# Performance work log

Measured on AMD Instinct MI355X. Metric: run time of the kernel, lower is better.

The kernel has to match this reference:

```python
import jax, jax.numpy as jnp
from jax import lax
import numpy as np

B, T, D_IN = 4, 1024, 8
D_MODEL, N_LAYERS, HORIZON, D_OUT = 512, 2, 24, 8
D_STATE, D_CONV, EXPAND = 64, 4, 2
D_INNER = EXPAND * D_MODEL
DT_RANK = -(-D_MODEL // 16)  # ceil(d_model/16) = 32
LN_EPS = 1e-5


def setup_inputs() -> dict:
    key = jax.random.key(0)
    ks = iter(jax.random.split(key, 24))
    rn = lambda shape, s: jax.random.normal(next(ks), shape, jnp.float32) * s
    A_log = jnp.tile(jnp.log(jnp.arange(1, D_STATE + 1, dtype=jnp.float32)), (N_LAYERS, D_INNER, 1))
    return {
        "x": rn((B, T, D_IN), 1.0),
        "W_in": rn((D_IN, D_MODEL), 0.3), "b_in": jnp.zeros((D_MODEL,), jnp.float32),
        "W_xz": rn((N_LAYERS, D_MODEL, 2 * D_INNER), 0.04),
        "conv_w": rn((N_LAYERS, D_INNER, D_CONV), 0.3), "conv_b": jnp.zeros((N_LAYERS, D_INNER), jnp.float32),
        "W_xproj": rn((N_LAYERS, D_INNER, DT_RANK + 2 * D_STATE), 0.03),
        "W_dt": rn((N_LAYERS, DT_RANK, D_INNER), 0.1), "b_dt": rn((N_LAYERS, D_INNER), 0.1) - 4.0,
        "A_log": A_log, "D_skip": jnp.ones((N_LAYERS, D_INNER), jnp.float32),
        "W_out": rn((N_LAYERS, D_INNER, D_MODEL), 0.03),
        "ln_g": jnp.ones((D_MODEL,), jnp.float32), "ln_b": jnp.zeros((D_MODEL,), jnp.float32),
        "W_h1": rn((D_MODEL, D_MODEL), 0.04), "b_h1": jnp.zeros((D_MODEL,), jnp.float32),
        "W_h2": rn((D_MODEL, HORIZON * D_OUT), 0.04), "b_h2": jnp.zeros((HORIZON * D_OUT,), jnp.float32),
    }


def mamba_block(h, Wxz, cw, cb, Wxp, Wdt, bdt, Alog, Dsk, Wout):
    # h: [B,T,d_model] -> [B,T,d_model]  (mamba-ssm Mamba block, no residual)
    xz = h @ Wxz                                   # [B,T,2*d_inner]
    xb, z = jnp.split(xz, 2, axis=-1)
    # depthwise causal conv over time
    xc = jnp.transpose(xb, (0, 2, 1))              # [B,d_inner,T]
    xc = lax.conv_general_dilated(xc, cw[:, None, :], (1,), [(D_CONV - 1, 0)],
                                  feature_group_count=D_INNER)
    xc = jax.nn.silu(xc + cb[None, :, None])
    xc = jnp.transpose(xc, (0, 2, 1))              # [B,T,d_inner]
    # input-dependent dt, B, C
    xdb = xc @ Wxp                                 # [B,T,dt_rank+2*d_state]
    dt_r = xdb[..., :DT_RANK]
    Bc = xdb[..., DT_RANK:DT_RANK + D_STATE]
    Cc = xdb[..., DT_RANK + D_STATE:]
    dt = jax.nn.softplus(dt_r @ Wdt + bdt)         # [B,T,d_inner]
    A = -jnp.exp(Alog)                             # [d_inner,d_state]

    def step(hst, ins):
        dt_t, B_t, C_t, x_t = ins                  # [B,d_inner],[B,N],[B,N],[B,d_inner]
        dA = jnp.exp(dt_t[..., None] * A)          # [B,d_inner,N]
        hst = dA * hst + dt_t[..., None] * B_t[:, None, :] * x_t[..., None]
        y = jnp.einsum('bdn,bn->bd', hst, C_t)
        return hst, y

    h0 = jnp.zeros((h.shape[0], D_INNER, D_STATE), h.dtype)
    xs = (jnp.transpose(dt, (1, 0, 2)), jnp.transpose(Bc, (1, 0, 2)),
          jnp.transpose(Cc, (1, 0, 2)), jnp.transpose(xc, (1, 0, 2)))
    _, ys = lax.scan(step, h0, xs)                 # ys: [T,B,d_inner]
    y = jnp.transpose(ys, (1, 0, 2)) + Dsk * xc
    y = y * jax.nn.silu(z)
    return y @ Wout


def reference(x, W_in, b_in, W_xz, conv_w, conv_b, W_xproj, W_dt, b_dt, A_log, D_skip,
              W_out, ln_g, ln_b, W_h1, b_h1, W_h2, b_h2):
    h = x @ W_in + b_in                            # [B,T,d_model]
    for i in range(N_LAYERS):
        h = mamba_block(h, W_xz[i], conv_w[i], conv_b[i], W_xproj[i], W_dt[i],
                        b_dt[i], A_log[i], D_skip[i], W_out[i])
    mu = jnp.mean(h, axis=-1, keepdims=True)
    var = jnp.mean(jnp.square(h - mu), axis=-1, keepdims=True)
    h = (h - mu) * lax.rsqrt(var + LN_EPS) * ln_g + ln_b
    last = h[:, -1, :]                             # [B,d_model]
    hid = jax.nn.gelu(last @ W_h1 + b_h1, approximate=False)
    yhat = hid @ W_h2 + b_h2                       # [B,horizon*d_out]
    return yhat.reshape(x.shape[0], HORIZON, D_OUT)
```

## Files before the change

kernel.cpp:

```cpp
#include <hip/hip_runtime.h>
#include <hip/hip_bf16.h>

static constexpr int kB      = 4;
static constexpr int kT      = 1024;
static constexpr int kDIN    = 8;
static constexpr int kDMODEL = 512;
static constexpr int kNLAYER = 2;
static constexpr int kHOR    = 24;
static constexpr int kDOUT   = 8;
static constexpr int kDSTATE = 64;
static constexpr int kDINNER = 1024;
static constexpr int kDTRANK = 32;
static constexpr int kXPROJ  = 160;
static constexpr int kXPAD   = 256;
static constexpr int kBT     = kB * kT;

typedef __bf16 bf16x8 __attribute__((ext_vector_type(8)));
typedef float  f32x4  __attribute__((ext_vector_type(4)));

__device__ __forceinline__ float silu_f(float x)     { return x / (1.f + __expf(-x)); }
__device__ __forceinline__ float softplus_f(float x) { return (x > 20.f) ? x : log1pf(__expf(x)); }
__device__ __forceinline__ float gelu_f(float x)     { return 0.5f * x * (1.f + erff(x * 0.70710678118654752f)); }

__device__ __forceinline__ void gld_lds16(const void* g, void* l) {
    __builtin_amdgcn_global_load_lds(
        (const __attribute__((address_space(1))) unsigned int*)g,
        (__attribute__((address_space(3))) unsigned int*)l, 16, 0, 0);
}

__device__ __forceinline__ float readlane_f(float v, int l) {
    return __int_as_float(__builtin_amdgcn_readlane(__float_as_int(v), l));
}
template<int CTRL>
__device__ __forceinline__ float dpp_mov(float v) {
    return __int_as_float(__builtin_amdgcn_update_dpp(
        0, __float_as_int(v), CTRL, 0xf, 0xf, false));
}

__global__ __launch_bounds__(256) void wtrans_kernel(
    const float* __restrict__ in, int K, int N, int in_lstride,
    __hip_bfloat16* __restrict__ out, int Kpad, int out_lstride)
{
    __shared__ float tile[32][33];
    const int tid = threadIdx.x;
    const int n0 = blockIdx.x * 32;
    const int k0 = blockIdx.y * 32;
    const float* inl = in + (size_t)blockIdx.z * in_lstride;
    __hip_bfloat16* outl = out + (size_t)blockIdx.z * out_lstride;

#pragma unroll
    for (int p = 0; p < 4; ++p) {
        int idx = p * 256 + tid;
        int ki = idx >> 5, ni = idx & 31;
        float v = 0.f;
        if (k0 + ki < K && n0 + ni < N) v = inl[(size_t)(k0 + ki) * N + n0 + ni];
        tile[ki][ni] = v;
    }
    __syncthreads();
#pragma unroll
    for (int p = 0; p < 4; ++p) {
        int idx = p * 256 + tid;
        int ni = idx >> 5, ki = idx & 31;
        outl[(size_t)(n0 + ni) * Kpad + k0 + ki] = __float2bfloat16(tile[ki][ni]);
    }
}

template<int MODE>
__global__ __launch_bounds__(256) void mfma_gemm_bt(
    const __hip_bfloat16* __restrict__ A, int lda,
    const __hip_bfloat16* __restrict__ BT, int ldb,
    const float* __restrict__ bias,
    float* __restrict__ C, int ldc,
    void* __restrict__ C2,
    int K)
{
    __shared__ __align__(16) __hip_bfloat16 sA[128][64];
    __shared__ __align__(16) __hip_bfloat16 sB[128][64];

    const int tid  = threadIdx.x;
    const int lane = tid & 63;
    const int w    = tid >> 6;
    const int wm   = w >> 1, wn = w & 1;
    const int m0   = blockIdx.y * 128;
    const int n0   = blockIdx.x * 128;

    f32x4 acc[4][4] = {};

    const int lrow = lane & 15;
    const int lk   = (lane >> 4) << 3;

    const int grow = tid >> 3;
    const int gcol = (tid & 7) * 8;
    char* ldsA = (char*)&sA[0][0] + w * 1024;
    char* ldsB = (char*)&sB[0][0] + w * 1024;

    for (int k0 = 0; k0 < K; k0 += 64) {
        __syncthreads();
#pragma unroll
        for (int p = 0; p < 4; ++p) {
            gld_lds16(A  + (size_t)(m0 + grow + p * 32) * lda + k0 + gcol, ldsA + p * 4096);
            gld_lds16(BT + (size_t)(n0 + grow + p * 32) * ldb + k0 + gcol, ldsB + p * 4096);
        }
        __syncthreads();
#pragma unroll
        for (int ks = 0; ks < 2; ++ks) {
            bf16x8 af[4], bfr[4];
#pragma unroll
            for (int i = 0; i < 4; ++i) {
                af[i]  = *reinterpret_cast<const bf16x8*>(&sA[wm * 64 + i * 16 + lrow][ks * 32 + lk]);
                bfr[i] = *reinterpret_cast<const bf16x8*>(&sB[wn * 64 + i * 16 + lrow][ks * 32 + lk]);
            }
#pragma unroll
            for (int i = 0; i < 4; ++i)
#pragma unroll
                for (int j = 0; j < 4; ++j)
                    acc[i][j] = __builtin_amdgcn_mfma_f32_16x16x32_bf16(af[i], bfr[j], acc[i][j], 0, 0, 0);
        }
    }

    const int crow = (lane >> 4) * 4;
    const int ccol = lane & 15;
#pragma unroll
    for (int i = 0; i < 4; ++i) {
#pragma unroll
        for (int j = 0; j < 4; ++j) {
#pragma unroll
            for (int r = 0; r < 4; ++r) {
                int row = m0 + wm * 64 + i * 16 + crow + r;
                int col = n0 + wn * 64 + j * 16 + ccol;
                float v = acc[i][j][r];
                if (MODE == 1) {
                    C[(size_t)row * ldc + col] = v;
                    ((__hip_bfloat16*)C2)[(size_t)row * ldc + col] = __float2bfloat16(v);
                } else if (MODE == 2) {
                    C[(size_t)row * ldc + col] = softplus_f(v + bias[col]);
                } else {
                    if (col < kDINNER)
                        ((__hip_bfloat16*)C)[(size_t)row * ldc + col] = __float2bfloat16(v);
                    else
                        ((__hip_bfloat16*)C2)[(size_t)row * ldc + (col - kDINNER)] =
                            __float2bfloat16(silu_f(v));
                }
            }
        }
    }
}

__global__ __launch_bounds__(256) void in_proj_kernel(
    const float* __restrict__ x, const float* __restrict__ W,
    const float* __restrict__ b,
    float* __restrict__ h, __hip_bfloat16* __restrict__ hb)
{
    int idx = blockIdx.x * 256 + threadIdx.x;
    int m = idx >> 9, n = idx & 511;
    float acc = b[n];
    const float* xr = x + m * kDIN;
#pragma unroll
    for (int k = 0; k < kDIN; ++k)
        acc = fmaf(xr[k], W[k * kDMODEL + n], acc);
    h[idx]  = acc;
    hb[idx] = __float2bfloat16(acc);
}

__global__ __launch_bounds__(256) void conv_silu_kernel(
    const __hip_bfloat16* __restrict__ xb,
    const float* __restrict__ cw, const float* __restrict__ cb,
    __hip_bfloat16* __restrict__ xc)
{
    int idx = blockIdx.x * 256 + threadIdx.x;
    int d   = idx & (kDINNER - 1);
    int bt  = idx >> 10;
    int t   = bt & (kT - 1);

    float4 wv = *reinterpret_cast<const float4*>(cw + d * 4);
    float acc = cb[d];
    const __hip_bfloat16* base = xb + (size_t)bt * kDINNER + d;
    if (t >= 3) {
        acc = fmaf(__bfloat162float(base[-3 * kDINNER]), wv.x, acc);
        acc = fmaf(__bfloat162float(base[-2 * kDINNER]), wv.y, acc);
        acc = fmaf(__bfloat162float(base[-1 * kDINNER]), wv.z, acc);
        acc = fmaf(__bfloat162float(base[0]),            wv.w, acc);
    } else {
        if (t >= 2) acc = fmaf(__bfloat162float(base[-2 * kDINNER]), wv.y, acc);
        if (t >= 1) acc = fmaf(__bfloat162float(base[-1 * kDINNER]), wv.z, acc);
        acc = fmaf(__bfloat162float(base[0]), wv.w, acc);
    }
    xc[idx] = __float2bfloat16(silu_f(acc));
}

__global__ __launch_bounds__(256, 4) void scan_kernel(
    const float* __restrict__ dt,
    const float* __restrict__ xdb,
    const __hip_bfloat16* __restrict__ xc,
    const __hip_bfloat16* __restrict__ zs,
    const float* __restrict__ Alog,
    const float* __restrict__ Dsk,
    __hip_bfloat16* __restrict__ yg)
{
    __shared__ __align__(16) float sBC[2][32][128];
    __shared__ float sY[2][32][4];

    const int tid  = threadIdx.x;
    const int lane = tid & 63;
    const int w    = tid >> 6;
    const int bb = blockIdx.x;
    const int b  = (bb & 7) >> 1;
    const int d0 = ((bb >> 3) + (bb & 1) * 128) * 4;
    const int d  = d0 + w;

    const float a2  = -__expf(Alog[d * kDSTATE + lane]) * 1.44269504f;
    const float dsk = Dsk[d];
    const size_t rowbase = (size_t)b * kT;
    float s = 0.f;

    auto stage = [&](int c, int buf) {
        const float* src = xdb + (rowbase + c * 32 + w * 8 + (lane >> 5)) * kXPAD
                               + kDTRANK + (lane & 31) * 4;
#pragma unroll
        for (int p = 0; p < 4; ++p)
            gld_lds16(src + p * 2 * kXPAD, &sBC[buf][w * 8 + p * 2][0]);
    };
    auto loadpair = [&](int pr, float& odt, float& oxc, float& odtx) {
        size_t row = rowbase + pr * 64 + lane;
        odt  = dt[row * kDINNER + d];
        oxc  = __bfloat162float(xc[row * kDINNER + d]);
        odtx = odt * oxc;
    };

    float vdt, vxc, vdtx;
    stage(0, 0);
    loadpair(0, vdt, vxc, vdtx);
    __syncthreads();

    for (int pr = 0; pr < kT / 64; ++pr) {
#pragma unroll
        for (int half = 0; half < 2; ++half) {
            const int c   = pr * 2 + half;
            const int buf = half;
            if (c + 1 < kT / 32) stage(c + 1, buf ^ 1);
            float ndt, nxc, ndtx;
            const bool ld = (half == 1) && (pr + 1 < kT / 64);
            if (ld) loadpair(pr + 1, ndt, nxc, ndtx);

            float yv[32];
#pragma unroll
            for (int i = 0; i < 32; ++i) {
                float Bv   = sBC[buf][i][lane];
                float Cv   = sBC[buf][i][64 + lane];
                float sdt  = readlane_f(vdt,  half * 32 + i);
                float sdtx = readlane_f(vdtx, half * 32 + i);
                float dA   = exp2f(sdt * a2);
                s = fmaf(dA, s, sdtx * Bv);
                yv[i] = s * Cv;
            }

#pragma unroll
            for (int m = 0; m < 16; ++m) {
                float av = yv[2 * m], bv = yv[2 * m + 1];
                float cv = (lane & 1) ? bv : av;
                float dv = (lane & 1) ? av : bv;
                yv[m] = cv + dpp_mov<0xB1>(dv);
            }
#pragma unroll
            for (int m = 0; m < 8; ++m) {
                float av = yv[2 * m], bv = yv[2 * m + 1];
                float cv = (lane & 2) ? bv : av;
                float dv = (lane & 2) ? av : bv;
                yv[m] = cv + dpp_mov<0x4E>(dv);
            }
#pragma unroll
            for (int j = 2; j < 5; ++j) {
                const int S = 1 << j;
#pragma unroll
                for (int m = 0; m < (32 >> (j + 1)); ++m) {
                    float av = yv[2 * m], bv = yv[2 * m + 1];
                    float cv = (lane & S) ? bv : av;
                    float dv = (lane & S) ? av : bv;
                    yv[m] = cv + __shfl_xor(dv, S, 64);
                }
            }
            float y = yv[0];
            y += __shfl_xor(y, 32, 64);

            if ((lane & 32) == half * 32)
                sY[buf][lane & 31][w] = fmaf(dsk, vxc, y);
            __syncthreads();

            if (tid < 128) {
                int r = tid >> 2, j2 = tid & 3;
                size_t g = (rowbase + c * 32 + r) * kDINNER + d0 + j2;
                yg[g] = __float2bfloat16(sY[buf][r][j2] * __bfloat162float(zs[g]));
            }
            if (ld) { vdt = ndt; vxc = nxc; vdtx = ndtx; }
        }
    }
}

template<int N, int KK, int ACT>
__global__ __launch_bounds__(256) void head_gemm(
    const float* __restrict__ A,
    const float* __restrict__ B,
    const float* __restrict__ bias,
    float* __restrict__ C)
{
    const int n = blockIdx.x * 64 + (threadIdx.x & 63);
    const int b = threadIdx.x >> 6;
    const float* a  = A + b * KK;
    const float* bp = B + n;
    float acc = 0.f;
#pragma unroll 16
    for (int k = 0; k < KK; ++k)
        acc = fmaf(a[k], bp[(size_t)k * N], acc);
    float v = acc + bias[n];
    if (ACT == 3) v = gelu_f(v);
    C[(size_t)b * N + n] = v;
}

__global__ __launch_bounds__(256) void ln_last_kernel(
    const float* __restrict__ h,
    const float* __restrict__ g, const float* __restrict__ be,
    float* __restrict__ out)
{
    __shared__ float sbuf[8];
    int b = blockIdx.x, tid = threadIdx.x;
    const float* row = h + (size_t)(b * kT + (kT - 1)) * kDMODEL;

    float v0 = row[tid], v1 = row[tid + 256];
    float s = v0 + v1;
    float q = v0 * v0 + v1 * v1;
#pragma unroll
    for (int m = 32; m >= 1; m >>= 1) {
        s += __shfl_xor(s, m, 64);
        q += __shfl_xor(q, m, 64);
    }
    int wid = tid >> 6;
    if ((tid & 63) == 0) { sbuf[wid] = s; sbuf[4 + wid] = q; }
    __syncthreads();
    if (tid == 0) {
        float S = 0.f, Q = 0.f;
        for (int i = 0; i < 4; ++i) { S += sbuf[i]; Q += sbuf[4 + i]; }
        sbuf[0] = S; sbuf[4] = Q;
    }
    __syncthreads();
    float mean = sbuf[0] * (1.f / kDMODEL);
    float var  = sbuf[4] * (1.f / kDMODEL) - mean * mean;
    float inv  = rsqrtf(var + 1e-5f);
    out[b * kDMODEL + tid]       = (v0 - mean) * inv * g[tid]       + be[tid];
    out[b * kDMODEL + tid + 256] = (v1 - mean) * inv * g[tid + 256] + be[tid + 256];
}

extern "C" void kernel_launch(void* const* d_in, const int* in_sizes, int n_in,
                              void* d_out, int out_size, void* d_ws, size_t ws_size,
                              hipStream_t stream)
{
    const float* x      = (const float*)d_in[0];
    const float* W_in   = (const float*)d_in[1];
    const float* b_in   = (const float*)d_in[2];
    const float* W_xz   = (const float*)d_in[3];
    const float* conv_w = (const float*)d_in[4];
    const float* conv_b = (const float*)d_in[5];
    const float* W_xp   = (const float*)d_in[6];
    const float* W_dt   = (const float*)d_in[7];
    const float* b_dt   = (const float*)d_in[8];
    const float* A_log  = (const float*)d_in[9];
    const float* D_skip = (const float*)d_in[10];
    const float* W_out  = (const float*)d_in[11];
    const float* ln_g   = (const float*)d_in[12];
    const float* ln_b   = (const float*)d_in[13];
    const float* W_h1   = (const float*)d_in[14];
    const float* b_h1   = (const float*)d_in[15];
    const float* W_h2   = (const float*)d_in[16];
    const float* b_h2   = (const float*)d_in[17];
    float* out = (float*)d_out;

    char* p = (char*)d_ws;
    auto alloc = [&](size_t bytes) { char* q = p; p += (bytes + 255) & ~(size_t)255; return q; };
    float*          h       = (float*)         alloc((size_t)kBT * kDMODEL * 4);
    __hip_bfloat16* h_bf    = (__hip_bfloat16*)alloc((size_t)kBT * kDMODEL * 2);
    __hip_bfloat16* xb_bf   = (__hip_bfloat16*)alloc((size_t)kBT * kDINNER * 2);
    __hip_bfloat16* z_bf    = (__hip_bfloat16*)alloc((size_t)kBT * kDINNER * 2);
    __hip_bfloat16* xc_bf   = (__hip_bfloat16*)alloc((size_t)kBT * kDINNER * 2);
    float*          xdb     = (float*)         alloc((size_t)kBT * kXPAD * 4);
    __hip_bfloat16* xdb_bf  = (__hip_bfloat16*)alloc((size_t)kBT * kXPAD * 2);
    float*          dtb     = (float*)         alloc((size_t)kBT * kDINNER * 4);
    __hip_bfloat16* ys_bf   = (__hip_bfloat16*)alloc((size_t)kBT * kDINNER * 2);
    __hip_bfloat16* wxz_bt  = (__hip_bfloat16*)alloc((size_t)2 * 2048 * 512 * 2);
    __hip_bfloat16* wxp_bt  = (__hip_bfloat16*)alloc((size_t)2 * 256 * 1024 * 2);
    __hip_bfloat16* wdt_bt  = (__hip_bfloat16*)alloc((size_t)2 * 1024 * 64 * 2);
    __hip_bfloat16* wout_bt = (__hip_bfloat16*)alloc((size_t)2 * 512 * 1024 * 2);
    float*          lnb     = (float*)         alloc(kB * kDMODEL * 4);
    float*          hid     = (float*)         alloc(kB * kDMODEL * 4);

    wtrans_kernel<<<dim3(64, 16, 2), 256, 0, stream>>>(W_xz, 512,  2048, 512 * 2048, wxz_bt,  512,  2048 * 512);
    wtrans_kernel<<<dim3(8,  32, 2), 256, 0, stream>>>(W_xp, 1024, 160,  1024 * 160, wxp_bt,  1024, 256 * 1024);
    wtrans_kernel<<<dim3(32, 2,  2), 256, 0, stream>>>(W_dt, 32,   1024, 32 * 1024,  wdt_bt,  64,   1024 * 64);
    wtrans_kernel<<<dim3(16, 32, 2), 256, 0, stream>>>(W_out, 1024, 512, 1024 * 512, wout_bt, 1024, 512 * 1024);

    in_proj_kernel<<<(kBT * kDMODEL) / 256, 256, 0, stream>>>(x, W_in, b_in, h, h_bf);

    for (int l = 0; l < kNLAYER; ++l) {
        const float* cw_l  = conv_w + (size_t)l * kDINNER * 4;
        const float* cb_l  = conv_b + (size_t)l * kDINNER;
        const float* bdt_l = b_dt   + (size_t)l * kDINNER;
        const float* Al_l  = A_log  + (size_t)l * kDINNER * kDSTATE;
        const float* Dsk_l = D_skip + (size_t)l * kDINNER;
        const __hip_bfloat16* wxz_l  = wxz_bt  + (size_t)l * 2048 * 512;
        const __hip_bfloat16* wxp_l  = wxp_bt  + (size_t)l * 256 * 1024;
        const __hip_bfloat16* wdt_l  = wdt_bt  + (size_t)l * 1024 * 64;
        const __hip_bfloat16* wout_l = wout_bt + (size_t)l * 512 * 1024;

        mfma_gemm_bt<4><<<dim3(16, 32), 256, 0, stream>>>(
            h_bf, kDMODEL, wxz_l, 512, nullptr, (float*)xb_bf, kDINNER, z_bf, kDMODEL);
        conv_silu_kernel<<<(kBT * kDINNER) / 256, 256, 0, stream>>>(xb_bf, cw_l, cb_l, xc_bf);
        mfma_gemm_bt<1><<<dim3(2, 32), 256, 0, stream>>>(
            xc_bf, kDINNER, wxp_l, 1024, nullptr, xdb, kXPAD, xdb_bf, kDINNER);
        mfma_gemm_bt<2><<<dim3(8, 32), 256, 0, stream>>>(
            xdb_bf, kXPAD, wdt_l, 64, bdt_l, dtb, kDINNER, nullptr, 64);
        scan_kernel<<<kB * kDINNER / 4, 256, 0, stream>>>(
            dtb, xdb, xc_bf, z_bf, Al_l, Dsk_l, ys_bf);
        mfma_gemm_bt<1><<<dim3(4, 32), 256, 0, stream>>>(
            ys_bf, kDINNER, wout_l, 1024, nullptr, h, kDMODEL, h_bf, kDINNER);
    }

    ln_last_kernel<<<kB, 256, 0, stream>>>(h, ln_g, ln_b, lnb);
    head_gemm<kDMODEL, kDMODEL, 3><<<kDMODEL / 64, 256, 0, stream>>>(lnb, W_h1, b_h1, hid);
    head_gemm<kHOR * kDOUT, kDMODEL, 0><<<(kHOR * kDOUT) / 64, 256, 0, stream>>>(hid, W_h2, b_h2, out);
}
```

Baseline: 528.5 us.

## Interleave B/C scan inputs, stage dt via LDS, vectorize conv and in-proj

The x-projection GEMM epilogue now writes B and C interleaved into a compact 128-wide fp32 buffer, so the scan reads both with a single float2 LDS load. The scan stages dt and dt*x per chunk into shared memory instead of using readlane broadcasts, and applies the D-skip and z gating per wave directly, dropping the extra sY round trip. The conv+silu and input-projection kernels are vectorized to 8 and 4 elements per thread. The aim is fewer scalar broadcasts and LDS round trips in the serial scan loop, plus wider memory accesses elsewhere. The cost is extra global reads of xc and z per wave in the scan.

```diff
diff --git a/kernel.cpp b/kernel.cpp
--- a/kernel.cpp
+++ b/kernel.cpp
@@ -28,9 +28,6 @@
         (__attribute__((address_space(3))) unsigned int*)l, 16, 0, 0);
 }
 
-__device__ __forceinline__ float readlane_f(float v, int l) {
-    return __int_as_float(__builtin_amdgcn_readlane(__float_as_int(v), l));
-}
 template<int CTRL>
 __device__ __forceinline__ float dpp_mov(float v) {
     return __int_as_float(__builtin_amdgcn_update_dpp(
@@ -134,12 +131,19 @@
                     ((__hip_bfloat16*)C2)[(size_t)row * ldc + col] = __float2bfloat16(v);
                 } else if (MODE == 2) {
                     C[(size_t)row * ldc + col] = softplus_f(v + bias[col]);
-                } else {
+                } else if (MODE == 4) {
                     if (col < kDINNER)
                         ((__hip_bfloat16*)C)[(size_t)row * ldc + col] = __float2bfloat16(v);
                     else
                         ((__hip_bfloat16*)C2)[(size_t)row * ldc + (col - kDINNER)] =
                             __float2bfloat16(silu_f(v));
+                } else {
+                    if (col < kDTRANK)
+                        ((__hip_bfloat16*)C2)[(size_t)row * kXPAD + col] = __float2bfloat16(v);
+                    else if (col < kDTRANK + kDSTATE)
+                        C[(size_t)row * 128 + (col - kDTRANK) * 2] = v;
+                    else if (col < kXPROJ)
+                        C[(size_t)row * 128 + (col - kDTRANK - kDSTATE) * 2 + 1] = v;
                 }
             }
         }
@@ -152,14 +156,23 @@
     float* __restrict__ h, __hip_bfloat16* __restrict__ hb)
 {
     int idx = blockIdx.x * 256 + threadIdx.x;
-    int m = idx >> 9, n = idx & 511;
-    float acc = b[n];
+    int n4 = (idx & 127) * 4;
+    int m  = idx >> 7;
+    float4 acc = *reinterpret_cast<const float4*>(b + n4);
     const float* xr = x + m * kDIN;
 #pragma unroll
-    for (int k = 0; k < kDIN; ++k)
-        acc = fmaf(xr[k], W[k * kDMODEL + n], acc);
-    h[idx]  = acc;
-    hb[idx] = __float2bfloat16(acc);
+    for (int k = 0; k < kDIN; ++k) {
+        float4 wv = *reinterpret_cast<const float4*>(W + k * kDMODEL + n4);
+        float xv = xr[k];
+        acc.x = fmaf(xv, wv.x, acc.x);
+        acc.y = fmaf(xv, wv.y, acc.y);
+        acc.z = fmaf(xv, wv.z, acc.z);
+        acc.w = fmaf(xv, wv.w, acc.w);
+    }
+    *reinterpret_cast<float4*>(h + (size_t)m * kDMODEL + n4) = acc;
+    __bf16 o4[4] = {(__bf16)acc.x, (__bf16)acc.y, (__bf16)acc.z, (__bf16)acc.w};
+    *reinterpret_cast<ushort4*>(hb + (size_t)m * kDMODEL + n4) =
+        *reinterpret_cast<ushort4*>(o4);
 }
 
 __global__ __launch_bounds__(256) void conv_silu_kernel(
@@ -168,29 +181,49 @@
     __hip_bfloat16* __restrict__ xc)
 {
     int idx = blockIdx.x * 256 + threadIdx.x;
-    int d   = idx & (kDINNER - 1);
-    int bt  = idx >> 10;
+    int dg  = (idx & 127) * 8;
+    int bt  = idx >> 7;
     int t   = bt & (kT - 1);
 
-    float4 wv = *reinterpret_cast<const float4*>(cw + d * 4);
-    float acc = cb[d];
-    const __hip_bfloat16* base = xb + (size_t)bt * kDINNER + d;
+    float4 wv[8];
+#pragma unroll
+    for (int k = 0; k < 8; ++k)
+        wv[k] = *reinterpret_cast<const float4*>(cw + (dg + k) * 4);
+
+    float acc[8];
+#pragma unroll
+    for (int k = 0; k < 8; ++k) acc[k] = cb[dg + k];
+
+    const __hip_bfloat16* base = xb + (size_t)bt * kDINNER + dg;
+    {
+        bf16x8 v = *reinterpret_cast<const bf16x8*>(base);
+#pragma unroll
+        for (int k = 0; k < 8; ++k) acc[k] = fmaf((float)v[k], wv[k].w, acc[k]);
+    }
+    if (t >= 1) {
+        bf16x8 v = *reinterpret_cast<const bf16x8*>(base - kDINNER);
+#pragma unroll
+        for (int k = 0; k < 8; ++k) acc[k] = fmaf((float)v[k], wv[k].z, acc[k]);
+    }
+    if (t >= 2) {
+        bf16x8 v = *reinterpret_cast<const bf16x8*>(base - 2 * kDINNER);
+#pragma unroll
+        for (int k = 0; k < 8; ++k) acc[k] = fmaf((float)v[k], wv[k].y, acc[k]);
+    }
     if (t >= 3) {
-        acc = fmaf(__bfloat162float(base[-3 * kDINNER]), wv.x, acc);
-        acc = fmaf(__bfloat162float(base[-2 * kDINNER]), wv.y, acc);
-        acc = fmaf(__bfloat162float(base[-1 * kDINNER]), wv.z, acc);
-        acc = fmaf(__bfloat162float(base[0]),            wv.w, acc);
-    } else {
-        if (t >= 2) acc = fmaf(__bfloat162float(base[-2 * kDINNER]), wv.y, acc);
-        if (t >= 1) acc = fmaf(__bfloat162float(base[-1 * kDINNER]), wv.z, acc);
-        acc = fmaf(__bfloat162float(base[0]), wv.w, acc);
-    }
-    xc[idx] = __float2bfloat16(silu_f(acc));
+        bf16x8 v = *reinterpret_cast<const bf16x8*>(base - 3 * kDINNER);
+#pragma unroll
+        for (int k = 0; k < 8; ++k) acc[k] = fmaf((float)v[k], wv[k].x, acc[k]);
+    }
+    bf16x8 o;
+#pragma unroll
+    for (int k = 0; k < 8; ++k) o[k] = (__bf16)silu_f(acc[k]);
+    *reinterpret_cast<bf16x8*>(xc + (size_t)bt * kDINNER + dg) = o;
 }
 
 __global__ __launch_bounds__(256, 4) void scan_kernel(
     const float* __restrict__ dt,
-    const float* __restrict__ xdb,
+    const float* __restrict__ xdbi,
     const __hip_bfloat16* __restrict__ xc,
     const __hip_bfloat16* __restrict__ zs,
     const float* __restrict__ Alog,
@@ -198,7 +231,7 @@
     __hip_bfloat16* __restrict__ yg)
 {
     __shared__ __align__(16) float sBC[2][32][128];
-    __shared__ float sY[2][32][4];
+    __shared__ __align__(8)  float sDT[2][32][4][2];
 
     const int tid  = threadIdx.x;
     const int lane = tid & 63;
@@ -213,86 +246,96 @@
     const size_t rowbase = (size_t)b * kT;
     float s = 0.f;
 
-    auto stage = [&](int c, int buf) {
-        const float* src = xdb + (rowbase + c * 32 + w * 8 + (lane >> 5)) * kXPAD
-                               + kDTRANK + (lane & 31) * 4;
+    auto stageBC = [&](int c, int buf) {
+        const float* src = xdbi + (rowbase + c * 32 + w * 8 + (lane >> 5)) * 128
+                                + (lane & 31) * 4;
 #pragma unroll
         for (int p = 0; p < 4; ++p)
-            gld_lds16(src + p * 2 * kXPAD, &sBC[buf][w * 8 + p * 2][0]);
+            gld_lds16(src + p * 2 * 128, &sBC[buf][w * 8 + p * 2][0]);
     };
-    auto loadpair = [&](int pr, float& odt, float& oxc, float& odtx) {
-        size_t row = rowbase + pr * 64 + lane;
-        odt  = dt[row * kDINNER + d];
-        oxc  = __bfloat162float(xc[row * kDINNER + d]);
-        odtx = odt * oxc;
+    const int sr = (tid & 127) >> 2, sj = tid & 3;
+    auto loadDT = [&](int c, float& odt, float& odx) {
+        if (tid < 128) {
+            size_t g = (rowbase + c * 32 + sr) * kDINNER + d0 + sj;
+            odt = dt[g];
+            odx = odt * (float)((const __bf16*)xc)[g];
+        }
     };
-
-    float vdt, vxc, vdtx;
-    stage(0, 0);
-    loadpair(0, vdt, vxc, vdtx);
+    auto writeDT = [&](int buf, float vdt, float vdx) {
+        if (tid < 128) {
+            sDT[buf][sr][sj][0] = vdt;
+            sDT[buf][sr][sj][1] = vdx;
+        }
+    };
+    auto loadEP = [&](int c, float& oxv, float& ozv) {
+        size_t g = (rowbase + c * 32 + (lane & 31)) * kDINNER + d;
+        oxv = (float)((const __bf16*)xc)[g];
+        ozv = (float)((const __bf16*)zs)[g];
+    };
+
+    float pdt = 0.f, pdx = 0.f, exv = 0.f, ezv = 0.f;
+    stageBC(0, 0);
+    loadDT(0, pdt, pdx);
+    loadEP(0, exv, ezv);
+    writeDT(0, pdt, pdx);
     __syncthreads();
 
-    for (int pr = 0; pr < kT / 64; ++pr) {
-#pragma unroll
-        for (int half = 0; half < 2; ++half) {
-            const int c   = pr * 2 + half;
-            const int buf = half;
-            if (c + 1 < kT / 32) stage(c + 1, buf ^ 1);
-            float ndt, nxc, ndtx;
-            const bool ld = (half == 1) && (pr + 1 < kT / 64);
-            if (ld) loadpair(pr + 1, ndt, nxc, ndtx);
-
-            float yv[32];
-#pragma unroll
-            for (int i = 0; i < 32; ++i) {
-                float Bv   = sBC[buf][i][lane];
-                float Cv   = sBC[buf][i][64 + lane];
-                float sdt  = readlane_f(vdt,  half * 32 + i);
-                float sdtx = readlane_f(vdtx, half * 32 + i);
-                float dA   = exp2f(sdt * a2);
-                s = fmaf(dA, s, sdtx * Bv);
-                yv[i] = s * Cv;
+    for (int c = 0; c < kT / 32; ++c) {
+        const int buf = c & 1;
+        float ndt = 0.f, ndx = 0.f, nxv = 0.f, nzv = 0.f;
+        const bool more = (c + 1 < kT / 32);
+        if (more) {
+            stageBC(c + 1, buf ^ 1);
+            loadDT(c + 1, ndt, ndx);
+            loadEP(c + 1, nxv, nzv);
+        }
+
+        float yv[32];
+#pragma unroll
+        for (int i = 0; i < 32; ++i) {
+            float2 bc = *reinterpret_cast<const float2*>(&sBC[buf][i][lane * 2]);
+            float2 dd = *reinterpret_cast<const float2*>(&sDT[buf][i][w][0]);
+            float dA = exp2f(dd.x * a2);
+            s = fmaf(dA, s, dd.y * bc.x);
+            yv[i] = s * bc.y;
+        }
+
+#pragma unroll
+        for (int m = 0; m < 16; ++m) {
+            float av = yv[2 * m], bv = yv[2 * m + 1];
+            float cv = (lane & 1) ? bv : av;
+            float dv = (lane & 1) ? av : bv;
+            yv[m] = cv + dpp_mov<0xB1>(dv);
+        }
+#pragma unroll
+        for (int m = 0; m < 8; ++m) {
+            float av = yv[2 * m], bv = yv[2 * m + 1];
+            float cv = (lane & 2) ? bv : av;
+            float dv = (lane & 2) ? av : bv;
+            yv[m] = cv + dpp_mov<0x4E>(dv);
+        }
+#pragma unroll
+        for (int j = 2; j < 5; ++j) {
+            const int S = 1 << j;
+#pragma unroll
+            for (int m = 0; m < (32 >> (j + 1)); ++m) {
+                float av = yv[2 * m], bv = yv[2 * m + 1];
+                float cv = (lane & S) ? bv : av;
+                float dv = (lane & S) ? av : bv;
+                yv[m] = cv + __shfl_xor(dv, S, 64);
             }
-
-#pragma unroll
-            for (int m = 0; m < 16; ++m) {
-                float av = yv[2 * m], bv = yv[2 * m + 1];
-                float cv = (lane & 1) ? bv : av;
-                float dv = (lane & 1) ? av : bv;
-                yv[m] = cv + dpp_mov<0xB1>(dv);
-            }
-#pragma unroll
-            for (int m = 0; m < 8; ++m) {
-                float av = yv[2 * m], bv = yv[2 * m + 1];
-                float cv = (lane & 2) ? bv : av;
-                float dv = (lane & 2) ? av : bv;
-                yv[m] = cv + dpp_mov<0x4E>(dv);
-            }
-#pragma unroll
-            for (int j = 2; j < 5; ++j) {
-                const int S = 1 << j;
-#pragma unroll
-                for (int m = 0; m < (32 >> (j + 1)); ++m) {
-                    float av = yv[2 * m], bv = yv[2 * m + 1];
-                    float cv = (lane & S) ? bv : av;
-                    float dv = (lane & S) ? av : bv;
-                    yv[m] = cv + __shfl_xor(dv, S, 64);
-                }
-            }
-            float y = yv[0];
-            y += __shfl_xor(y, 32, 64);
-
-            if ((lane & 32) == half * 32)
-                sY[buf][lane & 31][w] = fmaf(dsk, vxc, y);
-            __syncthreads();
-
-            if (tid < 128) {
-                int r = tid >> 2, j2 = tid & 3;
-                size_t g = (rowbase + c * 32 + r) * kDINNER + d0 + j2;
-                yg[g] = __float2bfloat16(sY[buf][r][j2] * __bfloat162float(zs[g]));
-            }
-            if (ld) { vdt = ndt; vxc = nxc; vdtx = ndtx; }
-        }
+        }
+        float y = yv[0];
+        y += __shfl_xor(y, 32, 64);
+
+        float yo = fmaf(dsk, exv, y) * ezv;
+        if (lane < 32) {
+            size_t g = (rowbase + c * 32 + lane) * kDINNER + d;
+            yg[g] = __float2bfloat16(yo);
+        }
+        if (more) writeDT(buf ^ 1, ndt, ndx);
+        __syncthreads();
+        exv = nxv; ezv = nzv;
     }
 }
 
@@ -380,7 +423,7 @@
     __hip_bfloat16* xb_bf   = (__hip_bfloat16*)alloc((size_t)kBT * kDINNER * 2);
     __hip_bfloat16* z_bf    = (__hip_bfloat16*)alloc((size_t)kBT * kDINNER * 2);
     __hip_bfloat16* xc_bf   = (__hip_bfloat16*)alloc((size_t)kBT * kDINNER * 2);
-    float*          xdb     = (float*)         alloc((size_t)kBT * kXPAD * 4);
+    float*          xdbi    = (float*)         alloc((size_t)kBT * 128 * 4);
     __hip_bfloat16* xdb_bf  = (__hip_bfloat16*)alloc((size_t)kBT * kXPAD * 2);
     float*          dtb     = (float*)         alloc((size_t)kBT * kDINNER * 4);
     __hip_bfloat16* ys_bf   = (__hip_bfloat16*)alloc((size_t)kBT * kDINNER * 2);
@@ -396,7 +439,7 @@
     wtrans_kernel<<<dim3(32, 2,  2), 256, 0, stream>>>(W_dt, 32,   1024, 32 * 1024,  wdt_bt,  64,   1024 * 64);
     wtrans_kernel<<<dim3(16, 32, 2), 256, 0, stream>>>(W_out, 1024, 512, 1024 * 512, wout_bt, 1024, 512 * 1024);
 
-    in_proj_kernel<<<(kBT * kDMODEL) / 256, 256, 0, stream>>>(x, W_in, b_in, h, h_bf);
+    in_proj_kernel<<<(kBT * 128) / 256, 256, 0, stream>>>(x, W_in, b_in, h, h_bf);
 
     for (int l = 0; l < kNLAYER; ++l) {
         const float* cw_l  = conv_w + (size_t)l * kDINNER * 4;
@@ -411,13 +454,13 @@
 
         mfma_gemm_bt<4><<<dim3(16, 32), 256, 0, stream>>>(
             h_bf, kDMODEL, wxz_l, 512, nullptr, (float*)xb_bf, kDINNER, z_bf, kDMODEL);
-        conv_silu_kernel<<<(kBT * kDINNER) / 256, 256, 0, stream>>>(xb_bf, cw_l, cb_l, xc_bf);
-        mfma_gemm_bt<1><<<dim3(2, 32), 256, 0, stream>>>(
-            xc_bf, kDINNER, wxp_l, 1024, nullptr, xdb, kXPAD, xdb_bf, kDINNER);
+        conv_silu_kernel<<<(kBT * 128) / 256, 256, 0, stream>>>(xb_bf, cw_l, cb_l, xc_bf);
+        mfma_gemm_bt<5><<<dim3(2, 32), 256, 0, stream>>>(
+            xc_bf, kDINNER, wxp_l, 1024, nullptr, xdbi, 128, xdb_bf, kDINNER);
         mfma_gemm_bt<2><<<dim3(8, 32), 256, 0, stream>>>(
             xdb_bf, kXPAD, wdt_l, 64, bdt_l, dtb, kDINNER, nullptr, 64);
         scan_kernel<<<kB * kDINNER / 4, 256, 0, stream>>>(
-            dtb, xdb, xc_bf, z_bf, Al_l, Dsk_l, ys_bf);
+            dtb, xdbi, xc_bf, z_bf, Al_l, Dsk_l, ys_bf);
         mfma_gemm_bt<1><<<dim3(4, 32), 256, 0, stream>>>(
             ys_bf, kDINNER, wout_l, 1024, nullptr, h, kDMODEL, h_bf, kDINNER);
     }
```

New measurement: 512.8 us. 1.03x faster.
